# Kernel optimization log

Measured on AMD Instinct MI355X. Metric: run time of the kernel, lower is better.

Reference implementation:

```python
import jax, jax.numpy as jnp
import numpy as np

B, N, H = 2, 160, 256
F = 512  # num_hidden_fc
C3 = 3 * H  # concatenated modality feature
C6 = 2 * C3  # pairwise feature


def setup_inputs() -> dict:
    key = jax.random.key(0)
    ks = jax.random.split(key, 16)
    s1 = 1.0 / np.sqrt(C6)
    s2 = 1.0 / np.sqrt(F)
    inp = {
        "geometry": jax.random.normal(ks[0], (B, N, H), jnp.float32),
        "appearance": jax.random.normal(ks[1], (B, N, H), jnp.float32),
        "content": jax.random.normal(ks[2], (B, N, H), jnp.float32),
    }
    for i, name in enumerate(["cell", "row", "col"]):
        inp[f"{name}_W1"] = jax.random.normal(ks[3 + 4 * i], (C6, F), jnp.float32) * s1
        inp[f"{name}_b1"] = jnp.zeros((F,), jnp.float32)
        inp[f"{name}_W2"] = jax.random.normal(ks[4 + 4 * i], (F, 2), jnp.float32) * s2
        inp[f"{name}_b2"] = jnp.zeros((2,), jnp.float32)
    return inp


def _head(x, W1, b1, W2, b2):
    h = jax.nn.relu(jnp.einsum("bpc,cf->bpf", x, W1) + b1)
    return jax.nn.softmax(jnp.einsum("bpf,fk->bpk", h, W2) + b2, axis=-1)


def reference(geometry, appearance, content,
              cell_W1, cell_b1, cell_W2, cell_b2,
              row_W1, row_b1, row_W2, row_b2,
              col_W1, col_b1, col_W2, col_b2):
    emb = jnp.concatenate([geometry, appearance, content], axis=-1)  # (B,N,3H)
    b, n, c = emb.shape
    # pairs[b,i,j] = concat(emb[b,j], emb[b,i])  (matches unsqueeze(1)/unsqueeze(2) order)
    e_j = jnp.broadcast_to(emb[:, None, :, :], (b, n, n, c))
    e_i = jnp.broadcast_to(emb[:, :, None, :], (b, n, n, c))
    emb_pairs = jnp.concatenate([e_j, e_i], axis=-1).reshape(b, n * n, 2 * c)
    cell_logits = _head(emb_pairs, cell_W1, cell_b1, cell_W2, cell_b2)
    row_logits = _head(emb_pairs, row_W1, row_b1, row_W2, row_b2)
    col_logits = _head(emb_pairs, col_W1, col_b1, col_W2, col_b2)
    return cell_logits, row_logits, col_logits, emb_pairs
```

## Files before the change

kernel.cpp:

```cpp
#include <hip/hip_runtime.h>

#define NB 2
#define NN 160
#define NPAIR (NN*NN)
#define OUT_PAIRS_OFF 307200

#define TOTAL_CHUNKS 19660800
#define TAIL_CHUNKS 245760
#define TAIL_START (TOTAL_CHUNKS - TAIL_CHUNKS)
#define PROJ_SCRATCH_OFF (OUT_PAIRS_OFF + 4*TAIL_START)

#define K1_PAIR_BLOCKS 42240
#define S1_CHUNKS (K1_PAIR_BLOCKS*256)
#define K2_PAIR_BLOCKS 33600

__device__ __forceinline__ void pairs_chunk(
    const float* __restrict__ geo, const float* __restrict__ app,
    const float* __restrict__ con, float4* __restrict__ outp, int idx)
{
    const int row = idx / 384;
    const int c   = idx - row * 384;
    const int b   = row / 25600;
    const int rem = row - b * 25600;
    const int i   = rem / 160;
    const int j   = rem - i * 160;

    int cc = c, pt = j;
    if (c >= 192) { pt = i; cc = c - 192; }
    const int m   = cc >> 6;
    const int off = cc & 63;
    const float* src = ((m == 0) ? geo : (m == 1) ? app : con)
                       + ((size_t)(b * 160 + pt)) * 256 + off * 4;

    outp[idx] = *(const float4*)src;
}

__global__ __launch_bounds__(256) void k1_proj_pairs(
    const float* __restrict__ geo, const float* __restrict__ app,
    const float* __restrict__ con,
    const float* __restrict__ w1c, const float* __restrict__ w1r,
    const float* __restrict__ w1l,
    const float* __restrict__ b1c, const float* __restrict__ b1r,
    const float* __restrict__ b1l,
    float* __restrict__ proj, float4* __restrict__ outp)
{
    const int tid = threadIdx.x;
    const int bid = blockIdx.x;

    if (bid >= 240) {
        pairs_chunk(geo, app, con, outp, (bid - 240) * 256 + tid);
        return;
    }

    __shared__ float As[64][17];
    __shared__ float Bs[16][68];

    const int m0 = (bid % 5) * 64;
    const int n0 = (bid / 5) * 64;
    const int t  = n0 >> 10;
    const int s  = (n0 >> 9) & 1;
    const int f0 = n0 & 511;

    const float* w1 = (t == 0) ? w1c : ((t == 1) ? w1r : w1l);
    const float* b1 = (t == 0) ? b1c : ((t == 1) ? b1r : b1l);

    const int ty = tid >> 4, tx = tid & 15;
    const int ar = tid >> 2, ac = (tid & 3) * 4;
    const int bk = tid >> 4, bn = (tid & 15) * 4;

    float acc[4][4] = {};

    for (int k0 = 0; k0 < 768; k0 += 16) {
        {
            const int c = k0 + ac;
            const int m = c >> 8, off = c & 255;
            const float* src = ((m == 0) ? geo : (m == 1) ? app : con)
                               + (size_t)(m0 + ar) * 256 + off;
            const float4 v = *(const float4*)src;
            As[ar][ac + 0] = v.x; As[ar][ac + 1] = v.y;
            As[ar][ac + 2] = v.z; As[ar][ac + 3] = v.w;
        }
        {
            const float4 v = *(const float4*)(
                w1 + (size_t)(s * 768 + k0 + bk) * 512 + f0 + bn);
            Bs[bk][bn + 0] = v.x; Bs[bk][bn + 1] = v.y;
            Bs[bk][bn + 2] = v.z; Bs[bk][bn + 3] = v.w;
        }
        __syncthreads();

        #pragma unroll
        for (int k = 0; k < 16; ++k) {
            const float4 b = *(const float4*)&Bs[k][tx * 4];
            const float a0 = As[ty * 4 + 0][k];
            const float a1 = As[ty * 4 + 1][k];
            const float a2 = As[ty * 4 + 2][k];
            const float a3 = As[ty * 4 + 3][k];
            acc[0][0] += a0 * b.x; acc[0][1] += a0 * b.y;
            acc[0][2] += a0 * b.z; acc[0][3] += a0 * b.w;
            acc[1][0] += a1 * b.x; acc[1][1] += a1 * b.y;
            acc[1][2] += a1 * b.z; acc[1][3] += a1 * b.w;
            acc[2][0] += a2 * b.x; acc[2][1] += a2 * b.y;
            acc[2][2] += a2 * b.z; acc[2][3] += a2 * b.w;
            acc[3][0] += a3 * b.x; acc[3][1] += a3 * b.y;
            acc[3][2] += a3 * b.z; acc[3][3] += a3 * b.w;
        }
        __syncthreads();
    }

    float4 bias = {0.f, 0.f, 0.f, 0.f};
    if (s == 0) bias = *(const float4*)&b1[f0 + tx * 4];

    #pragma unroll
    for (int r = 0; r < 4; ++r) {
        float4 o;
        o.x = acc[r][0] + bias.x; o.y = acc[r][1] + bias.y;
        o.z = acc[r][2] + bias.z; o.w = acc[r][3] + bias.w;
        *(float4*)&proj[(size_t)((t * 2 + s) * 320 + m0 + ty * 4 + r) * 512
                        + f0 + tx * 4] = o;
    }
}

__global__ __launch_bounds__(256) void k2_heads_pairs(
    const float* __restrict__ geo, const float* __restrict__ app,
    const float* __restrict__ con,
    const float* __restrict__ proj,
    const float* __restrict__ w2c, const float* __restrict__ b2c,
    const float* __restrict__ w2r, const float* __restrict__ b2r,
    const float* __restrict__ w2l, const float* __restrict__ b2l,
    float* __restrict__ out, float4* __restrict__ outp)
{
    const int tid = threadIdx.x;
    const int bid = blockIdx.x;

    if (bid >= 200) {
        pairs_chunk(geo, app, con, outp,
                    S1_CHUNKS + (bid - 200) * 256 + tid);
        return;
    }

    __shared__ float P1s[16][516];
    __shared__ float P2s[16][516];
    __shared__ float w2s[1024];
    __shared__ float b2s[2];

    const int b   = bid / 100;
    const int rem = bid - b * 100;
    const int it  = rem / 10;
    const int jt  = rem - it * 10;
    const int i0 = it * 16, j0 = jt * 16;
    const int ii = tid >> 4, jj = tid & 15;

    #pragma unroll
    for (int t = 0; t < 3; ++t) {
        const float* w2 = (t == 0) ? w2c : ((t == 1) ? w2r : w2l);
        const float* b2 = (t == 0) ? b2c : ((t == 1) ? b2r : b2l);

        for (int u = tid; u < 4096; u += 256) {
            const int tile = u >> 11;
            const int r    = (u >> 7) & 15;
            const int f4   = u & 127;
            const int p    = b * 160 + (tile ? (i0 + r) : (j0 + r));
            const float4 v = *(const float4*)(
                proj + ((size_t)((t * 2 + tile) * 320 + p)) * 512 + f4 * 4);
            float* dst = tile ? &P2s[r][f4 * 4] : &P1s[r][f4 * 4];
            *(float4*)dst = v;
        }
        if (tid < 256)
            *(float4*)&w2s[tid * 4] = *(const float4*)(w2 + tid * 4);
        if (tid < 2) b2s[tid] = b2[tid];
        __syncthreads();

        float a0 = b2s[0], a1 = b2s[1];
        for (int f = 0; f < 512; f += 4) {
            const float4 p1 = *(const float4*)&P1s[jj][f];
            const float4 p2 = *(const float4*)&P2s[ii][f];
            const float4 wA = *(const float4*)&w2s[f * 2];
            const float4 wB = *(const float4*)&w2s[f * 2 + 4];
            const float h0 = fmaxf(p1.x + p2.x, 0.f);
            const float h1 = fmaxf(p1.y + p2.y, 0.f);
            const float h2 = fmaxf(p1.z + p2.z, 0.f);
            const float h3 = fmaxf(p1.w + p2.w, 0.f);
            a0 += h0 * wA.x + h1 * wA.z + h2 * wB.x + h3 * wB.z;
            a1 += h0 * wA.y + h1 * wA.w + h2 * wB.y + h3 * wB.w;
        }

        const float mx = fmaxf(a0, a1);
        const float e0 = __expf(a0 - mx);
        const float e1 = __expf(a1 - mx);
        const float rs = 1.f / (e0 + e1);

        const int pr = b * 25600 + (i0 + ii) * 160 + (j0 + jj);
        float2 o; o.x = e0 * rs; o.y = e1 * rs;
        ((float2*)out)[t * 51200 + pr] = o;
        __syncthreads();
    }
}

__global__ __launch_bounds__(256) void k3_pairs_tail(
    const float* __restrict__ geo, const float* __restrict__ app,
    const float* __restrict__ con, float4* __restrict__ outp)
{
    pairs_chunk(geo, app, con, outp,
                TAIL_START + blockIdx.x * 256 + threadIdx.x);
}

extern "C" void kernel_launch(void* const* d_in, const int* in_sizes, int n_in,
                              void* d_out, int out_size, void* d_ws, size_t ws_size,
                              hipStream_t stream)
{
    const float* geo = (const float*)d_in[0];
    const float* app = (const float*)d_in[1];
    const float* con = (const float*)d_in[2];
    const float* w1c = (const float*)d_in[3];
    const float* b1c = (const float*)d_in[4];
    const float* w2c = (const float*)d_in[5];
    const float* b2c = (const float*)d_in[6];
    const float* w1r = (const float*)d_in[7];
    const float* b1r = (const float*)d_in[8];
    const float* w2r = (const float*)d_in[9];
    const float* b2r = (const float*)d_in[10];
    const float* w1l = (const float*)d_in[11];
    const float* b1l = (const float*)d_in[12];
    const float* w2l = (const float*)d_in[13];
    const float* b2l = (const float*)d_in[14];

    float* out = (float*)d_out;

    float* proj = out + PROJ_SCRATCH_OFF;
    float4* outp = (float4*)(out + OUT_PAIRS_OFF);

    k1_proj_pairs<<<240 + K1_PAIR_BLOCKS, 256, 0, stream>>>(
        geo, app, con, w1c, w1r, w1l, b1c, b1r, b1l, proj, outp);

    k2_heads_pairs<<<200 + K2_PAIR_BLOCKS, 256, 0, stream>>>(
        geo, app, con, proj, w2c, b2c, w2r, b2r, w2l, b2l, out, outp);

    k3_pairs_tail<<<960, 256, 0, stream>>>(geo, app, con, outp);
}
```

Before: 429.5 us.

## Use workspace for projection scratch, drop tail kernel, transpose A tile

When a large enough workspace is provided, the projection scratch moves there instead of the end of the output buffer. The heads kernel then writes all remaining pair chunks itself and the third tail-copy launch is skipped, saving one kernel launch and its dependency. The GEMM A tile is also stored transposed in shared memory so each thread reads its four A values with one float4 load instead of four scalar loads. If no workspace is available, it falls back to the old three-kernel path.

```diff
diff --git a/kernel.cpp b/kernel.cpp
--- a/kernel.cpp
+++ b/kernel.cpp
@@ -6,13 +6,15 @@
 #define OUT_PAIRS_OFF 307200
 
 #define TOTAL_CHUNKS 19660800
+#define PROJ_BYTES 3932160
 #define TAIL_CHUNKS 245760
 #define TAIL_START (TOTAL_CHUNKS - TAIL_CHUNKS)
 #define PROJ_SCRATCH_OFF (OUT_PAIRS_OFF + 4*TAIL_START)
 
 #define K1_PAIR_BLOCKS 42240
 #define S1_CHUNKS (K1_PAIR_BLOCKS*256)
-#define K2_PAIR_BLOCKS 33600
+#define K2_PAIR_BLOCKS_WS   34560
+#define K2_PAIR_BLOCKS_TAIL 33600
 
 __device__ __forceinline__ void pairs_chunk(
     const float* __restrict__ geo, const float* __restrict__ app,
@@ -52,7 +54,7 @@
         return;
     }
 
-    __shared__ float As[64][17];
+    __shared__ float Ast[16][76];
     __shared__ float Bs[16][68];
 
     const int m0 = (bid % 5) * 64;
@@ -77,8 +79,8 @@
             const float* src = ((m == 0) ? geo : (m == 1) ? app : con)
                                + (size_t)(m0 + ar) * 256 + off;
             const float4 v = *(const float4*)src;
-            As[ar][ac + 0] = v.x; As[ar][ac + 1] = v.y;
-            As[ar][ac + 2] = v.z; As[ar][ac + 3] = v.w;
+            Ast[ac + 0][ar] = v.x; Ast[ac + 1][ar] = v.y;
+            Ast[ac + 2][ar] = v.z; Ast[ac + 3][ar] = v.w;
         }
         {
             const float4 v = *(const float4*)(
@@ -91,18 +93,15 @@
         #pragma unroll
         for (int k = 0; k < 16; ++k) {
             const float4 b = *(const float4*)&Bs[k][tx * 4];
-            const float a0 = As[ty * 4 + 0][k];
-            const float a1 = As[ty * 4 + 1][k];
-            const float a2 = As[ty * 4 + 2][k];
-            const float a3 = As[ty * 4 + 3][k];
-            acc[0][0] += a0 * b.x; acc[0][1] += a0 * b.y;
-            acc[0][2] += a0 * b.z; acc[0][3] += a0 * b.w;
-            acc[1][0] += a1 * b.x; acc[1][1] += a1 * b.y;
-            acc[1][2] += a1 * b.z; acc[1][3] += a1 * b.w;
-            acc[2][0] += a2 * b.x; acc[2][1] += a2 * b.y;
-            acc[2][2] += a2 * b.z; acc[2][3] += a2 * b.w;
-            acc[3][0] += a3 * b.x; acc[3][1] += a3 * b.y;
-            acc[3][2] += a3 * b.z; acc[3][3] += a3 * b.w;
+            const float4 a = *(const float4*)&Ast[k][ty * 4];
+            acc[0][0] += a.x * b.x; acc[0][1] += a.x * b.y;
+            acc[0][2] += a.x * b.z; acc[0][3] += a.x * b.w;
+            acc[1][0] += a.y * b.x; acc[1][1] += a.y * b.y;
+            acc[1][2] += a.y * b.z; acc[1][3] += a.y * b.w;
+            acc[2][0] += a.z * b.x; acc[2][1] += a.z * b.y;
+            acc[2][2] += a.z * b.z; acc[2][3] += a.z * b.w;
+            acc[3][0] += a.w * b.x; acc[3][1] += a.w * b.y;
+            acc[3][2] += a.w * b.z; acc[3][3] += a.w * b.w;
         }
         __syncthreads();
     }
@@ -165,8 +164,7 @@
             float* dst = tile ? &P2s[r][f4 * 4] : &P1s[r][f4 * 4];
             *(float4*)dst = v;
         }
-        if (tid < 256)
-            *(float4*)&w2s[tid * 4] = *(const float4*)(w2 + tid * 4);
+        *(float4*)&w2s[tid * 4] = *(const float4*)(w2 + tid * 4);
         if (tid < 2) b2s[tid] = b2[tid];
         __syncthreads();
 
@@ -225,15 +223,18 @@
     const float* b2l = (const float*)d_in[14];
 
     float* out = (float*)d_out;
-
-    float* proj = out + PROJ_SCRATCH_OFF;
     float4* outp = (float4*)(out + OUT_PAIRS_OFF);
+
+    const bool use_ws = (d_ws != nullptr) && (ws_size >= (size_t)PROJ_BYTES);
+    float* proj = use_ws ? (float*)d_ws : (out + PROJ_SCRATCH_OFF);
 
     k1_proj_pairs<<<240 + K1_PAIR_BLOCKS, 256, 0, stream>>>(
         geo, app, con, w1c, w1r, w1l, b1c, b1r, b1l, proj, outp);
 
-    k2_heads_pairs<<<200 + K2_PAIR_BLOCKS, 256, 0, stream>>>(
+    const int k2_pairs = use_ws ? K2_PAIR_BLOCKS_WS : K2_PAIR_BLOCKS_TAIL;
+    k2_heads_pairs<<<200 + k2_pairs, 256, 0, stream>>>(
         geo, app, con, proj, w2c, b2c, w2r, b2r, w2l, b2l, out, outp);
 
-    k3_pairs_tail<<<960, 256, 0, stream>>>(geo, app, con, outp);
-}
+    if (!use_ws)
+        k3_pairs_tail<<<960, 256, 0, stream>>>(geo, app, con, outp);
+}
```

Result: faster. 418.5 us (-2.6%).
